# Kernel tuning notes

Hardware: AMD Instinct MI355X
Metric: run time of the kernel (lower is better)

Reference implementation:

```python
import jax, jax.numpy as jnp
import numpy as np

NEG_SLOPE = 0.2

def setup_inputs() -> dict:
    key = jax.random.key(0)
    k1, k2, k3, k4, k5 = jax.random.split(key, 5)
    B, N, IN_DIM, H, D = 4, 2048, 256, 4, 64
    x = jax.random.normal(k1, (B, N, IN_DIM), dtype=jnp.float32)
    A_mask = jax.random.randint(k2, (N, N), 0, 2, dtype=jnp.int32)
    # xavier-like scaled params
    W = jax.random.normal(k3, (IN_DIM, H * D), dtype=jnp.float32) * (1.0 / np.sqrt(IN_DIM))
    a_src = jax.random.normal(k4, (H, D), dtype=jnp.float32) * (1.0 / np.sqrt(D))
    a_dst = jax.random.normal(k5, (H, D), dtype=jnp.float32) * (1.0 / np.sqrt(D))
    return {"x": x, "A_mask": A_mask, "W": W, "a_src": a_src, "a_dst": a_dst}

def reference(x, A_mask, W, a_src, a_dst):
    B, N, _ = x.shape
    H, D = a_src.shape
    # h: [B, N, H, D]
    h = (x @ W).reshape(B, N, H, D)
    # per-node attention scores: [B, N, H]
    src = jnp.einsum('bnhd,hd->bnh', h, a_src)
    dst = jnp.einsum('bnhd,hd->bnh', h, a_dst)
    # logits: [B, H, N, N] = src_i + dst_j, then leaky_relu
    logits = src.transpose(0, 2, 1)[:, :, :, None] + dst.transpose(0, 2, 1)[:, :, None, :]
    logits = jnp.where(logits >= 0, logits, NEG_SLOPE * logits)
    # mask (shared across batch and heads)
    logits = jnp.where(A_mask[None, None, :, :] == 0, -jnp.inf, logits)
    attn = jax.nn.softmax(logits, axis=-1)  # [B, H, N, N]
    # weighted sum over neighbors
    out = jnp.einsum('bhnm,bmhd->bnhd', attn, h).reshape(B, N, H * D)
    return jax.nn.elu(out)
```

## Files before the change

### kernel.cpp

```cpp
#include <hip/hip_runtime.h>

typedef float  f32x4 __attribute__((ext_vector_type(4)));
typedef short  s16x8 __attribute__((ext_vector_type(8)));

__device__ __forceinline__ unsigned short f2bf(float f){
    unsigned int u = __float_as_uint(f);
    u = u + 0x7FFFu + ((u >> 16) & 1u);
    return (unsigned short)(u >> 16);
}

__global__ void k_wt(const float* __restrict__ W, unsigned short* __restrict__ WT){
    int c = blockIdx.x, k = threadIdx.x;
    WT[c*256 + k] = f2bf(W[k*256 + c]);
}

__global__ void k_bits(const int* __restrict__ mask, unsigned long long* __restrict__ bits64){
    int i = blockIdx.x;
    int wave = threadIdx.x >> 6, lane = threadIdx.x & 63;
    for (int c = wave; c < 32; c += 4){
        int v = mask[i*2048 + c*64 + lane];
        unsigned long long b = __ballot(v != 0);
        if (lane == 0) bits64[i*32 + c] = b;
    }
}

__global__ __launch_bounds__(256) void k_gemm(const float* __restrict__ x,
        const unsigned short* __restrict__ WT,
        const float* __restrict__ a_src, const float* __restrict__ a_dst,
        unsigned short* __restrict__ hTt, float* __restrict__ src, float* __restrict__ dst){
    const int wave = threadIdx.x >> 6, lane = threadIdx.x & 63;
    const int q = lane >> 4, t = lane & 15;
    const int m0 = blockIdx.x*64 + wave*16;
    const int head = blockIdx.y;
    f32x4 acc[4] = {{0,0,0,0},{0,0,0,0},{0,0,0,0},{0,0,0,0}};
    const int row = m0 + t;
    for (int k = 0; k < 256; k += 32){
        int kk = k + q*8;
        const float* xp = x + row*256 + kk;
        f32x4 x0 = *reinterpret_cast<const f32x4*>(xp);
        f32x4 x1 = *reinterpret_cast<const f32x4*>(xp + 4);
        s16x8 a;
#pragma unroll
        for (int j = 0; j < 4; j++){ a[j] = (short)f2bf(x0[j]); a[j+4] = (short)f2bf(x1[j]); }
#pragma unroll
        for (int dblk = 0; dblk < 4; dblk++){
            s16x8 bfr = *reinterpret_cast<const s16x8*>(WT + (head*64 + dblk*16 + t)*256 + kk);
            acc[dblk] = __builtin_amdgcn_mfma_f32_16x16x32_bf16(a, bfr, acc[dblk], 0, 0, 0);
        }
    }
    const int b = m0 >> 11;
    const int bh = b*4 + head;
    const int jb = (m0 & 2047) >> 4;
    float as_[4], ad_[4];
#pragma unroll
    for (int dblk = 0; dblk < 4; dblk++){
        as_[dblk] = a_src[head*64 + dblk*16 + t];
        ad_[dblk] = a_dst[head*64 + dblk*16 + t];
    }
#pragma unroll
    for (int reg = 0; reg < 4; reg++){
        float sv = acc[0][reg]*as_[0] + acc[1][reg]*as_[1] + acc[2][reg]*as_[2] + acc[3][reg]*as_[3];
        float dv = acc[0][reg]*ad_[0] + acc[1][reg]*ad_[1] + acc[2][reg]*ad_[2] + acc[3][reg]*ad_[3];
#pragma unroll
        for (int off = 1; off < 16; off <<= 1){
            sv += __shfl_xor(sv, off);
            dv += __shfl_xor(dv, off);
        }
        if (t == 0){
            int n = (m0 & 2047) + q*4 + reg;
            src[bh*2048 + n] = sv;
            dst[bh*2048 + n] = dv;
        }
    }
#pragma unroll
    for (int dblk = 0; dblk < 4; dblk++){
        int d = dblk*16 + t;
#pragma unroll
        for (int reg = 0; reg < 4; reg++){
            int jj = q*4 + reg;
            hTt[((bh*128 + jb)*64 + d)*16 + jj] = f2bf(acc[dblk][reg]);
        }
    }
}

__device__ __forceinline__ s16x8 make_p(unsigned int bs, float vsrc, f32x4 d0, f32x4 d1, float NEGINF){
    float e[8];
#pragma unroll
    for (int jj = 0; jj < 8; jj++){
        float dvv = (jj < 4) ? d0[jj] : d1[jj-4];
        float lg = vsrc + dvv;
        lg = fmaxf(lg, 0.2f*lg);
        lg = ((bs >> jj) & 1u) ? lg : NEGINF;
        e[jj] = __expf(lg);
    }
    union { unsigned int u[4]; s16x8 s; } pk;
#pragma unroll
    for (int p = 0; p < 4; p++)
        pk.u[p] = __builtin_amdgcn_perm(__float_as_uint(e[2*p+1]), __float_as_uint(e[2*p]), 0x07060302u);
    return pk.s;
}

__global__ __launch_bounds__(256, 4) void k_attn(const unsigned short* __restrict__ hTt,
        const unsigned int* __restrict__ bits, const float* __restrict__ src,
        const float* __restrict__ dst, float* __restrict__ out){
    __shared__ float accL[4][16][64];
    __shared__ float Sl[4][16];
    const int bh = blockIdx.x;
    const int b = bh >> 2, head = bh & 3;
    const int wave = threadIdx.x >> 6, lane = threadIdx.x & 63;
    const int q = lane >> 4, t = lane & 15, q8 = q*8;
    const int i0 = blockIdx.y*32;
    const float NEGINF = -__builtin_inff();
    const float vsrc0 = src[bh*2048 + i0 + t];
    const float vsrc1 = src[bh*2048 + i0 + 16 + t];
    const unsigned int* bR0 = bits + (i0 + t)*64 + wave*16;
    const unsigned int* bR1 = bR0 + 16*64;
    const float* dR = dst + bh*2048 + wave*512 + q8;
    const unsigned short* vB = hTt + bh*131072 + wave*32768 + (q>>1)*1024 + (q&1)*8 + t*16;
    f32x4 a00={0,0,0,0},a01={0,0,0,0},a02={0,0,0,0},a03={0,0,0,0};
    f32x4 a10={0,0,0,0},a11={0,0,0,0},a12={0,0,0,0},a13={0,0,0,0};
    f32x4 s0acc={0,0,0,0}, s1acc={0,0,0,0};
    s16x8 ones;
#pragma unroll
    for (int j = 0; j < 8; j++) ones[j] = (short)0x3F80;
    for (int it = 0; it < 16; ++it){
        const unsigned short* vp = vB + it*2048;
        s16x8 h0 = *reinterpret_cast<const s16x8*>(vp);
        s16x8 h1 = *reinterpret_cast<const s16x8*>(vp + 256);
        s16x8 h2 = *reinterpret_cast<const s16x8*>(vp + 512);
        s16x8 h3 = *reinterpret_cast<const s16x8*>(vp + 768);
        unsigned int bs0 = bR0[it] >> q8;
        unsigned int bs1 = bR1[it] >> q8;
        f32x4 d0 = *reinterpret_cast<const f32x4*>(dR + it*32);
        f32x4 d1 = *reinterpret_cast<const f32x4*>(dR + it*32 + 4);
        s16x8 p0 = make_p(bs0, vsrc0, d0, d1, NEGINF);
        s16x8 p1 = make_p(bs1, vsrc1, d0, d1, NEGINF);
        a00 = __builtin_amdgcn_mfma_f32_16x16x32_bf16(p0, h0, a00, 0,0,0);
        a01 = __builtin_amdgcn_mfma_f32_16x16x32_bf16(p0, h1, a01, 0,0,0);
        a02 = __builtin_amdgcn_mfma_f32_16x16x32_bf16(p0, h2, a02, 0,0,0);
        a03 = __builtin_amdgcn_mfma_f32_16x16x32_bf16(p0, h3, a03, 0,0,0);
        s0acc = __builtin_amdgcn_mfma_f32_16x16x32_bf16(p0, ones, s0acc, 0,0,0);
        a10 = __builtin_amdgcn_mfma_f32_16x16x32_bf16(p1, h0, a10, 0,0,0);
        a11 = __builtin_amdgcn_mfma_f32_16x16x32_bf16(p1, h1, a11, 0,0,0);
        a12 = __builtin_amdgcn_mfma_f32_16x16x32_bf16(p1, h2, a12, 0,0,0);
        a13 = __builtin_amdgcn_mfma_f32_16x16x32_bf16(p1, h3, a13, 0,0,0);
        s1acc = __builtin_amdgcn_mfma_f32_16x16x32_bf16(p1, ones, s1acc, 0,0,0);
    }
#pragma unroll
    for (int half = 0; half < 2; half++){
        f32x4 c0 = half ? a10 : a00;
        f32x4 c1 = half ? a11 : a01;
        f32x4 c2 = half ? a12 : a02;
        f32x4 c3 = half ? a13 : a03;
        f32x4 sc = half ? s1acc : s0acc;
        if (half) __syncthreads();
#pragma unroll
        for (int reg = 0; reg < 4; reg++){
            int r = q*4 + reg;
            accL[wave][r][ 0 + t] = c0[reg];
            accL[wave][r][16 + t] = c1[reg];
            accL[wave][r][32 + t] = c2[reg];
            accL[wave][r][48 + t] = c3[reg];
        }
        if (t == 0){
#pragma unroll
            for (int reg = 0; reg < 4; reg++) Sl[wave][q*4 + reg] = sc[reg];
        }
        __syncthreads();
        const int tid = threadIdx.x;
        const int row = tid >> 4;
        const int d   = (tid & 15) * 4;
        f32x4 v0 = *reinterpret_cast<const f32x4*>(&accL[0][row][d]);
        f32x4 v1 = *reinterpret_cast<const f32x4*>(&accL[1][row][d]);
        f32x4 v2 = *reinterpret_cast<const f32x4*>(&accL[2][row][d]);
        f32x4 v3 = *reinterpret_cast<const f32x4*>(&accL[3][row][d]);
        float Ssum = Sl[0][row] + Sl[1][row] + Sl[2][row] + Sl[3][row];
        float rS = 1.0f / Ssum;
        f32x4 v;
#pragma unroll
        for (int c = 0; c < 4; c++){
            float vv = (v0[c] + v1[c] + v2[c] + v3[c]) * rS;
            v[c] = vv > 0.f ? vv : (__expf(vv) - 1.0f);
        }
        *reinterpret_cast<f32x4*>(out + (b*2048 + i0 + half*16 + row)*256 + head*64 + d) = v;
    }
}

extern "C" void kernel_launch(void* const* d_in, const int* in_sizes, int n_in,
                              void* d_out, int out_size, void* d_ws, size_t ws_size,
                              hipStream_t stream) {
    const float* x     = (const float*)d_in[0];
    const int*   Amask = (const int*)d_in[1];
    const float* W     = (const float*)d_in[2];
    const float* a_src = (const float*)d_in[3];
    const float* a_dst = (const float*)d_in[4];
    float* out = (float*)d_out;

    char* ws = (char*)d_ws;
    unsigned short*     hTt  = (unsigned short*)(ws);
    unsigned long long* bits = (unsigned long long*)(ws + (4u<<20));
    unsigned short*     WT   = (unsigned short*)(ws + (4u<<20) + (512u<<10));
    float*              src  = (float*)(ws + (4u<<20) + (640u<<10));
    float*              dst  = (float*)(ws + (4u<<20) + (768u<<10));

    hipLaunchKernelGGL(k_wt,   dim3(256),     dim3(256), 0, stream, W, WT);
    hipLaunchKernelGGL(k_bits, dim3(2048),    dim3(256), 0, stream, Amask, bits);
    hipLaunchKernelGGL(k_gemm, dim3(128, 4),  dim3(256), 0, stream, x, WT, a_src, a_dst, hTt, src, dst);
    hipLaunchKernelGGL(k_attn, dim3(16, 64),  dim3(256), 0, stream, hTt, (const unsigned int*)bits, src, dst, out);
}
```

Baseline: 123.0 us.

## Factor exp of leaky-relu logits into per-node exponentials and widen attention tiles

New measurement: 148.4 us. 1.21x slower.

```diff
diff --git a/kernel.cpp b/kernel.cpp
--- a/kernel.cpp
+++ b/kernel.cpp
@@ -9,25 +9,28 @@
     return (unsigned short)(u >> 16);
 }
 
-__global__ void k_wt(const float* __restrict__ W, unsigned short* __restrict__ WT){
-    int c = blockIdx.x, k = threadIdx.x;
-    WT[c*256 + k] = f2bf(W[k*256 + c]);
-}
-
-__global__ void k_bits(const int* __restrict__ mask, unsigned long long* __restrict__ bits64){
-    int i = blockIdx.x;
-    int wave = threadIdx.x >> 6, lane = threadIdx.x & 63;
-    for (int c = wave; c < 32; c += 4){
-        int v = mask[i*2048 + c*64 + lane];
-        unsigned long long b = __ballot(v != 0);
-        if (lane == 0) bits64[i*32 + c] = b;
+__global__ void k_prep(const float* __restrict__ W, unsigned short* __restrict__ WT,
+                       const int* __restrict__ mask, unsigned long long* __restrict__ bits64){
+    int bid = blockIdx.x;
+    if (bid < 2048){
+        int i = bid;
+        int wave = threadIdx.x >> 6, lane = threadIdx.x & 63;
+        for (int c = wave; c < 32; c += 4){
+            int v = mask[i*2048 + c*64 + lane];
+            unsigned long long b = __ballot(v != 0);
+            if (lane == 0) bits64[i*32 + c] = b;
+        }
+    } else {
+        int c = bid - 2048, k = threadIdx.x;
+        WT[c*256 + k] = f2bf(W[k*256 + c]);
     }
 }
 
 __global__ __launch_bounds__(256) void k_gemm(const float* __restrict__ x,
         const unsigned short* __restrict__ WT,
         const float* __restrict__ a_src, const float* __restrict__ a_dst,
-        unsigned short* __restrict__ hTt, float* __restrict__ src, float* __restrict__ dst){
+        unsigned short* __restrict__ hTt, float* __restrict__ E1a, float* __restrict__ E2a,
+        float* __restrict__ F1a, float* __restrict__ F2a){
     const int wave = threadIdx.x >> 6, lane = threadIdx.x & 63;
     const int q = lane >> 4, t = lane & 15;
     const int m0 = blockIdx.x*64 + wave*16;
@@ -68,8 +71,10 @@
         }
         if (t == 0){
             int n = (m0 & 2047) + q*4 + reg;
-            src[bh*2048 + n] = sv;
-            dst[bh*2048 + n] = dv;
+            E1a[bh*2048 + n] = __expf(sv);
+            E2a[bh*2048 + n] = __expf(0.2f*sv);
+            F1a[bh*2048 + n] = __expf(dv);
+            F2a[bh*2048 + n] = __expf(0.2f*dv);
         }
     }
 #pragma unroll
@@ -83,43 +88,53 @@
     }
 }
 
-__device__ __forceinline__ s16x8 make_p(unsigned int bs, float vsrc, f32x4 d0, f32x4 d1, float NEGINF){
-    float e[8];
+__device__ __forceinline__ s16x8 make_p2(unsigned int bs, float e1, float e2,
+        f32x4 f1lo, f32x4 f1hi, f32x4 f2lo, f32x4 f2hi){
+    float p[8];
 #pragma unroll
     for (int jj = 0; jj < 8; jj++){
-        float dvv = (jj < 4) ? d0[jj] : d1[jj-4];
-        float lg = vsrc + dvv;
-        lg = fmaxf(lg, 0.2f*lg);
-        lg = ((bs >> jj) & 1u) ? lg : NEGINF;
-        e[jj] = __expf(lg);
+        float F1 = (jj < 4) ? f1lo[jj] : f1hi[jj-4];
+        float F2 = (jj < 4) ? f2lo[jj] : f2hi[jj-4];
+        float m1 = e1*F1, m2 = e2*F2;
+        float pp = (m1 >= 1.0f) ? m1 : m2;
+        p[jj] = ((bs >> jj) & 1u) ? pp : 0.0f;
     }
     union { unsigned int u[4]; s16x8 s; } pk;
 #pragma unroll
-    for (int p = 0; p < 4; p++)
-        pk.u[p] = __builtin_amdgcn_perm(__float_as_uint(e[2*p+1]), __float_as_uint(e[2*p]), 0x07060302u);
+    for (int z = 0; z < 4; z++)
+        pk.u[z] = __builtin_amdgcn_perm(__float_as_uint(p[2*z+1]), __float_as_uint(p[2*z]), 0x07060302u);
     return pk.s;
 }
 
 __global__ __launch_bounds__(256, 4) void k_attn(const unsigned short* __restrict__ hTt,
-        const unsigned int* __restrict__ bits, const float* __restrict__ src,
-        const float* __restrict__ dst, float* __restrict__ out){
+        const unsigned int* __restrict__ bits, const float* __restrict__ E1a,
+        const float* __restrict__ E2a, const float* __restrict__ F1a,
+        const float* __restrict__ F2a, float* __restrict__ out){
     __shared__ float accL[4][16][64];
     __shared__ float Sl[4][16];
     const int bh = blockIdx.x;
     const int b = bh >> 2, head = bh & 3;
     const int wave = threadIdx.x >> 6, lane = threadIdx.x & 63;
     const int q = lane >> 4, t = lane & 15, q8 = q*8;
-    const int i0 = blockIdx.y*32;
-    const float NEGINF = -__builtin_inff();
-    const float vsrc0 = src[bh*2048 + i0 + t];
-    const float vsrc1 = src[bh*2048 + i0 + 16 + t];
-    const unsigned int* bR0 = bits + (i0 + t)*64 + wave*16;
-    const unsigned int* bR1 = bR0 + 16*64;
-    const float* dR = dst + bh*2048 + wave*512 + q8;
+    const int i0 = blockIdx.y*64;
+    float E1[4], E2[4];
+#pragma unroll
+    for (int f = 0; f < 4; f++){
+        E1[f] = E1a[bh*2048 + i0 + f*16 + t];
+        E2[f] = E2a[bh*2048 + i0 + f*16 + t];
+    }
+    const unsigned int* bR = bits + (i0 + t)*64 + wave*16;
+    const float* F1p = F1a + bh*2048 + wave*512 + q8;
+    const float* F2p = F2a + bh*2048 + wave*512 + q8;
     const unsigned short* vB = hTt + bh*131072 + wave*32768 + (q>>1)*1024 + (q&1)*8 + t*16;
-    f32x4 a00={0,0,0,0},a01={0,0,0,0},a02={0,0,0,0},a03={0,0,0,0};
-    f32x4 a10={0,0,0,0},a11={0,0,0,0},a12={0,0,0,0},a13={0,0,0,0};
-    f32x4 s0acc={0,0,0,0}, s1acc={0,0,0,0};
+    f32x4 acc[4][4];
+    f32x4 sacc[4];
+#pragma unroll
+    for (int f = 0; f < 4; f++){
+        sacc[f] = (f32x4){0.f,0.f,0.f,0.f};
+#pragma unroll
+        for (int d = 0; d < 4; d++) acc[f][d] = (f32x4){0.f,0.f,0.f,0.f};
+    }
     s16x8 ones;
 #pragma unroll
     for (int j = 0; j < 8; j++) ones[j] = (short)0x3F80;
@@ -129,42 +144,35 @@
         s16x8 h1 = *reinterpret_cast<const s16x8*>(vp + 256);
         s16x8 h2 = *reinterpret_cast<const s16x8*>(vp + 512);
         s16x8 h3 = *reinterpret_cast<const s16x8*>(vp + 768);
-        unsigned int bs0 = bR0[it] >> q8;
-        unsigned int bs1 = bR1[it] >> q8;
-        f32x4 d0 = *reinterpret_cast<const f32x4*>(dR + it*32);
-        f32x4 d1 = *reinterpret_cast<const f32x4*>(dR + it*32 + 4);
-        s16x8 p0 = make_p(bs0, vsrc0, d0, d1, NEGINF);
-        s16x8 p1 = make_p(bs1, vsrc1, d0, d1, NEGINF);
-        a00 = __builtin_amdgcn_mfma_f32_16x16x32_bf16(p0, h0, a00, 0,0,0);
-        a01 = __builtin_amdgcn_mfma_f32_16x16x32_bf16(p0, h1, a01, 0,0,0);
-        a02 = __builtin_amdgcn_mfma_f32_16x16x32_bf16(p0, h2, a02, 0,0,0);
-        a03 = __builtin_amdgcn_mfma_f32_16x16x32_bf16(p0, h3, a03, 0,0,0);
-        s0acc = __builtin_amdgcn_mfma_f32_16x16x32_bf16(p0, ones, s0acc, 0,0,0);
-        a10 = __builtin_amdgcn_mfma_f32_16x16x32_bf16(p1, h0, a10, 0,0,0);
-        a11 = __builtin_amdgcn_mfma_f32_16x16x32_bf16(p1, h1, a11, 0,0,0);
-        a12 = __builtin_amdgcn_mfma_f32_16x16x32_bf16(p1, h2, a12, 0,0,0);
-        a13 = __builtin_amdgcn_mfma_f32_16x16x32_bf16(p1, h3, a13, 0,0,0);
-        s1acc = __builtin_amdgcn_mfma_f32_16x16x32_bf16(p1, ones, s1acc, 0,0,0);
-    }
-#pragma unroll
-    for (int half = 0; half < 2; half++){
-        f32x4 c0 = half ? a10 : a00;
-        f32x4 c1 = half ? a11 : a01;
-        f32x4 c2 = half ? a12 : a02;
-        f32x4 c3 = half ? a13 : a03;
-        f32x4 sc = half ? s1acc : s0acc;
-        if (half) __syncthreads();
+        f32x4 f1lo = *reinterpret_cast<const f32x4*>(F1p + it*32);
+        f32x4 f1hi = *reinterpret_cast<const f32x4*>(F1p + it*32 + 4);
+        f32x4 f2lo = *reinterpret_cast<const f32x4*>(F2p + it*32);
+        f32x4 f2hi = *reinterpret_cast<const f32x4*>(F2p + it*32 + 4);
+#pragma unroll
+        for (int f = 0; f < 4; f++){
+            unsigned int bs = bR[f*1024 + it] >> q8;
+            s16x8 pf = make_p2(bs, E1[f], E2[f], f1lo, f1hi, f2lo, f2hi);
+            acc[f][0] = __builtin_amdgcn_mfma_f32_16x16x32_bf16(pf, h0, acc[f][0], 0,0,0);
+            acc[f][1] = __builtin_amdgcn_mfma_f32_16x16x32_bf16(pf, h1, acc[f][1], 0,0,0);
+            acc[f][2] = __builtin_amdgcn_mfma_f32_16x16x32_bf16(pf, h2, acc[f][2], 0,0,0);
+            acc[f][3] = __builtin_amdgcn_mfma_f32_16x16x32_bf16(pf, h3, acc[f][3], 0,0,0);
+            sacc[f]   = __builtin_amdgcn_mfma_f32_16x16x32_bf16(pf, ones, sacc[f], 0,0,0);
+        }
+    }
+#pragma unroll
+    for (int f = 0; f < 4; f++){
+        if (f) __syncthreads();
 #pragma unroll
         for (int reg = 0; reg < 4; reg++){
             int r = q*4 + reg;
-            accL[wave][r][ 0 + t] = c0[reg];
-            accL[wave][r][16 + t] = c1[reg];
-            accL[wave][r][32 + t] = c2[reg];
-            accL[wave][r][48 + t] = c3[reg];
+            accL[wave][r][ 0 + t] = acc[f][0][reg];
+            accL[wave][r][16 + t] = acc[f][1][reg];
+            accL[wave][r][32 + t] = acc[f][2][reg];
+            accL[wave][r][48 + t] = acc[f][3][reg];
         }
         if (t == 0){
 #pragma unroll
-            for (int reg = 0; reg < 4; reg++) Sl[wave][q*4 + reg] = sc[reg];
+            for (int reg = 0; reg < 4; reg++) Sl[wave][q*4 + reg] = sacc[f][reg];
         }
         __syncthreads();
         const int tid = threadIdx.x;
@@ -182,7 +190,7 @@
             float vv = (v0[c] + v1[c] + v2[c] + v3[c]) * rS;
             v[c] = vv > 0.f ? vv : (__expf(vv) - 1.0f);
         }
-        *reinterpret_cast<f32x4*>(out + (b*2048 + i0 + half*16 + row)*256 + head*64 + d) = v;
+        *reinterpret_cast<f32x4*>(out + (b*2048 + i0 + f*16 + row)*256 + head*64 + d) = v;
     }
 }
 
@@ -200,11 +208,12 @@
     unsigned short*     hTt  = (unsigned short*)(ws);
     unsigned long long* bits = (unsigned long long*)(ws + (4u<<20));
     unsigned short*     WT   = (unsigned short*)(ws + (4u<<20) + (512u<<10));
-    float*              src  = (float*)(ws + (4u<<20) + (640u<<10));
-    float*              dst  = (float*)(ws + (4u<<20) + (768u<<10));
-
-    hipLaunchKernelGGL(k_wt,   dim3(256),     dim3(256), 0, stream, W, WT);
-    hipLaunchKernelGGL(k_bits, dim3(2048),    dim3(256), 0, stream, Amask, bits);
-    hipLaunchKernelGGL(k_gemm, dim3(128, 4),  dim3(256), 0, stream, x, WT, a_src, a_dst, hTt, src, dst);
-    hipLaunchKernelGGL(k_attn, dim3(16, 64),  dim3(256), 0, stream, hTt, (const unsigned int*)bits, src, dst, out);
-}
+    float*              E1a  = (float*)(ws + (4u<<20) + (640u<<10));
+    float*              E2a  = (float*)(ws + (4u<<20) + (768u<<10));
+    float*              F1a  = (float*)(ws + (4u<<20) + (896u<<10));
+    float*              F2a  = (float*)(ws + (4u<<20) + (1024u<<10));
+
+    hipLaunchKernelGGL(k_prep, dim3(2304),    dim3(256), 0, stream, W, WT, Amask, (unsigned long long*)bits);
+    hipLaunchKernelGGL(k_gemm, dim3(128, 4),  dim3(256), 0, stream, x, WT, a_src, a_dst, hTt, E1a, E2a, F1a, F2a);
+    hipLaunchKernelGGL(k_attn, dim3(16, 32),  dim3(256), 0, stream, hTt, (const unsigned int*)bits, E1a, E2a, F1a, F2a, out);
+}
```
